# Performance work log

Hardware: AMD Instinct MI355X
Metric: run time of the kernel (lower is better)

The kernel has to match this reference:

```python
import jax, jax.numpy as jnp
import numpy as np

TAG_THR = 0.1
MIN_HEIGHT = 0.0
PULL_WEIGHT = 1.0
PUSH_WEIGHT = 1.0
EPS = 1e-6


def _bbox_iou(boxes):
    # boxes: [N,4] -> IoU [N,N] (standard, no +1 offset; heights in the loss
    # are also computed without +1)
    x1, y1, x2, y2 = boxes[:, 0], boxes[:, 1], boxes[:, 2], boxes[:, 3]
    area = (x2 - x1) * (y2 - y1)
    iw = jnp.clip(jnp.minimum(x2[:, None], x2[None, :]) - jnp.maximum(x1[:, None], x1[None, :]), 0.0)
    ih = jnp.clip(jnp.minimum(y2[:, None], y2[None, :]) - jnp.maximum(y1[:, None], y1[None, :]), 0.0)
    inter = iw * ih
    union = area[:, None] + area[None, :] - inter
    return inter / jnp.maximum(union, 1e-12)


def _single_image(pred, gt_inds, proposals):
    # pred [N,D], gt_inds [N] int, proposals [N,5]
    N = pred.shape[0]
    heights = proposals[:, 3] - proposals[:, 1]
    valid = (gt_inds >= 0) & (heights > MIN_HEIGHT)
    scores = proposals[:, 4]
    iou = _bbox_iou(proposals[:, :4])  # [N,N]

    def step(state, _):
        alive, tot_pull, tot_push, pull_cnt, push_cnt = state
        active = jnp.sum(alive) >= 2  # pop i; if nothing remains, the torch loop breaks
        # i = highest-scoring remaining proposal (greedy, score-sorted)
        i = jnp.argmax(jnp.where(alive, scores, -jnp.inf))
        rem = alive.at[i].set(False)
        overlap = (iou[i] > 0.0) & rem
        diff = jnp.mean((pred - pred[i]) ** 2, axis=1)  # [N]
        check = diff < TAG_THR
        same = gt_inds == gt_inds[i]
        pull_m = overlap & same & ~check
        push_m = overlap & ~same & check
        pn = jnp.sum(pull_m)
        qn = jnp.sum(push_m)
        pull_l = jnp.sum(jnp.where(pull_m, diff * scores, 0.0)) / jnp.maximum(pn, 1).astype(diff.dtype)
        push_l = jnp.sum(jnp.where(push_m, jnp.exp(-diff) * scores, 0.0)) / jnp.maximum(qn, 1).astype(diff.dtype)
        add_pull = active & (pn > 0)
        add_push = active & (qn > 0)
        tot_pull = tot_pull + jnp.where(add_pull, pull_l, 0.0)
        tot_push = tot_push + jnp.where(add_push, push_l, 0.0)
        pull_cnt = pull_cnt + add_pull.astype(jnp.float32)
        push_cnt = push_cnt + add_push.astype(jnp.float32)
        # suppress everything overlapping i whose tag is already close (diff < thr)
        new_alive = rem & ~(overlap & check)
        alive = jnp.where(active, new_alive, alive)
        return (alive, tot_pull, tot_push, pull_cnt, push_cnt), None

    z = jnp.float32(0.0)
    init = (valid, z, z, z, z)
    (_, tot_pull, tot_push, pull_cnt, push_cnt), _ = jax.lax.scan(step, init, None, length=N)
    pull = tot_pull / (pull_cnt + EPS)
    push = tot_push / (push_cnt + EPS)
    return push, pull


def setup_inputs() -> dict:
    key = jax.random.key(0)
    k1, k2, k3, k4, k5, k6, k7 = jax.random.split(key, 7)
    IMGS, N, D = 4, 2000, 4
    pred = jax.random.normal(k1, (IMGS, N, D), dtype=jnp.float32)
    gt_inds = jax.random.randint(k2, (IMGS, N), 0, 50, dtype=jnp.int32)
    x1 = jax.random.uniform(k3, (IMGS, N), minval=0.0, maxval=800.0)
    y1 = jax.random.uniform(k4, (IMGS, N), minval=0.0, maxval=800.0)
    w = jax.random.uniform(k5, (IMGS, N), minval=8.0, maxval=128.0)
    h = jax.random.uniform(k6, (IMGS, N), minval=8.0, maxval=128.0)
    score = jax.random.uniform(k7, (IMGS, N), minval=0.0, maxval=1.0)
    proposals = jnp.stack([x1, y1, x1 + w, y1 + h, score], axis=-1).astype(jnp.float32)
    gt_bboxes = jax.random.uniform(jax.random.fold_in(key, 9), (IMGS, 20, 4), dtype=jnp.float32)
    return {"pred": pred, "gt_inds": gt_inds, "proposals": proposals, "gt_bboxes": gt_bboxes}


def reference(pred, gt_inds, proposals, gt_bboxes):
    # gt_bboxes is accepted by the torch forward but never used in the loss math.
    push, pull = jax.vmap(_single_image)(pred, gt_inds, proposals)  # per-image scalars
    img_num = pred.shape[0]
    push_loss = jnp.sum(push) / img_num * PUSH_WEIGHT
    pull_loss = jnp.sum(pull) / img_num * PULL_WEIGHT
    return push_loss, pull_loss
```

## Files before the change

kernel.cpp:

```cpp
#include <hip/hip_runtime.h>
#include <stdint.h>

#define BLOCK 256
#define KMAX 8
#define NWAVES (BLOCK / 64)
#define S2 2048
#define NW 32
#define NCH 32
#define SPB 16
#define PB (S2 / SPB)
#define RB (S2 / BLOCK)
#define PCAP 65536
#define LDSP 6144
#define EFF_INF 0x7FFFFFFF

__device__ inline int rank_of(const unsigned long long* ss, int j) {
    int jw = j >> 6, jb = j & 63;
    int rk = __popcll(ss[jw] & (jb ? (~0ull >> (64 - jb)) : 0ull));
    for (int w = 0; w < jw; ++w) rk += __popcll(ss[w]);
    return rk;
}

__global__ __launch_bounds__(BLOCK) void rankcount_kernel(
    const float* __restrict__ proposals,
    int* __restrict__ partial, int* __restrict__ pcnt, int N, int imgs)
{
    const int bi = blockIdx.x, bj = blockIdx.y, img = blockIdx.z;
    const int t = threadIdx.x;
    if (bi == 0 && bj == 0 && t == 0) pcnt[img] = 0;
    const float* P = proposals + (size_t)img * N * 5;
    __shared__ unsigned sj[BLOCK];
    const int jbase = bj * BLOCK;
    {
        int j = jbase + t;
        sj[t] = (j < N) ? __float_as_uint(P[j*5 + 4]) : 0u;
    }
    __syncthreads();
    const int i = bi * BLOCK + t;
    if (i >= N) return;
    const unsigned my = __float_as_uint(P[i*5 + 4]);
    int p = 0;
    const uint4* s4 = (const uint4*)sj;
#pragma unroll
    for (int q = 0; q < BLOCK/4; ++q) {
        uint4 v = s4[q];
        int jj = jbase + q*4;
        p += (int)((v.x > my) | ((v.x == my) & (jj + 0 < i)));
        p += (int)((v.y > my) | ((v.y == my) & (jj + 1 < i)));
        p += (int)((v.z > my) | ((v.z == my) & (jj + 2 < i)));
        p += (int)((v.w > my) | ((v.w == my) & (jj + 3 < i)));
    }
    partial[((size_t)(img*RB + bj))*S2 + i] = p;
}

__global__ __launch_bounds__(BLOCK) void rankscatter_kernel(
    const float* __restrict__ pred, const int* __restrict__ gt_inds,
    const float* __restrict__ proposals, const int* __restrict__ partial,
    float* __restrict__ soa, int* __restrict__ sgt, int N, int imgs)
{
    const int img = blockIdx.y, t = threadIdx.x;
    const int i = blockIdx.x * BLOCK + t;
    const size_t stride = (size_t)imgs * S2;
    const size_t base   = (size_t)img * S2;

    if (i >= N) {
        if (i < S2) {
#pragma unroll
            for (int a = 0; a < 9; ++a) soa[(size_t)a*stride + base + i] = 0.f;
            sgt[base + i] = -1;
        }
        return;
    }

    const float* P = proposals + (size_t)img * N * 5;
    const float* E = pred      + (size_t)img * N * 4;
    const int*   G = gt_inds   + (size_t)img * N;

    const float p0 = P[i*5+0], p1 = P[i*5+1], p2 = P[i*5+2],
                p3 = P[i*5+3], p4 = P[i*5+4];
    const float q0 = E[i*4+0], q1 = E[i*4+1], q2 = E[i*4+2], q3 = E[i*4+3];
    const int   gg = G[i];

    int p = 0;
#pragma unroll
    for (int b = 0; b < RB; ++b)
        p += partial[((size_t)(img*RB + b))*S2 + i];

    soa[0*stride + base + p] = p0;
    soa[1*stride + base + p] = p1;
    soa[2*stride + base + p] = p2;
    soa[3*stride + base + p] = p3;
    soa[4*stride + base + p] = p4;
    soa[5*stride + base + p] = q0;
    soa[6*stride + base + p] = q1;
    soa[7*stride + base + p] = q2;
    soa[8*stride + base + p] = q3;
    sgt[base + p] = gg;
}

__global__ __launch_bounds__(BLOCK) void suppairs_kernel(
    const float* __restrict__ soa, unsigned* __restrict__ pairs,
    int* __restrict__ pcnt, int N, int imgs)
{
    const int ic = blockIdx.x, jc = blockIdx.y, img = blockIdx.z;
    if (ic < jc) return;
    const int t = threadIdx.x, wave = t >> 6, lane = t & 63;
    const size_t stride = (size_t)imgs * S2, base = (size_t)img * S2;
    __shared__ float si[8][64];
    for (int idx = t; idx < 512; idx += BLOCK) {
        int f = idx >> 6, e = idx & 63;
        int a = (f < 4) ? f : f + 1;
        si[f][e] = soa[(size_t)a*stride + base + ic*64 + e];
    }
    __syncthreads();
    const int j = jc*64 + lane;
    const float jx1 = soa[0*stride+base+j], jy1 = soa[1*stride+base+j];
    const float jx2 = soa[2*stride+base+j], jy2 = soa[3*stride+base+j];
    const float j0  = soa[5*stride+base+j], j1  = soa[6*stride+base+j];
    const float j2  = soa[7*stride+base+j], j3  = soa[8*stride+base+j];
    const bool jin = (j < N);
    unsigned* PL = pairs + (size_t)img * PCAP;
    for (int ii = 0; ii < 16; ++ii) {
        int il = wave*16 + ii;
        int i  = ic*64 + il;
        float bx1 = si[0][il], by1 = si[1][il], bx2 = si[2][il], by2 = si[3][il];
        float f0  = si[4][il], f1  = si[5][il], f2  = si[6][il], f3  = si[7][il];
        bool s = false;
        if (jin && i < N && i > j) {
            float iw = fminf(jx2, bx2) - fmaxf(jx1, bx1);
            float ih = fminf(jy2, by2) - fmaxf(jy1, by1);
            if (iw > 0.f && ih > 0.f) {
                float d0 = j0-f0, d1 = j1-f1, d2 = j2-f2, d3 = j3-f3;
                float diff = 0.25f*(d0*d0 + d1*d1 + d2*d2 + d3*d3);
                s = diff < 0.1f;
            }
        }
        unsigned long long m = __ballot(s);
        if (m) {
            int leader = __ffsll((unsigned long long)m) - 1;
            int basei = 0;
            if (lane == leader) basei = atomicAdd(&pcnt[img], __popcll(m));
            basei = __shfl(basei, leader);
            if (s) {
                int idx = basei + __popcll(m & ((lane == 0) ? 0ull : (~0ull >> (64 - lane))));
                if (idx < PCAP) PL[idx] = ((unsigned)j << 11) | (unsigned)i;
            }
        }
    }
}

__global__ __launch_bounds__(64) void greedy_kernel(
    const unsigned* __restrict__ pairs, const int* __restrict__ pcnt,
    const int* __restrict__ sgt, const float* __restrict__ soa,
    unsigned long long* __restrict__ selw_out, int imgs)
{
    const int img = blockIdx.x, l = threadIdx.x;
    const size_t stride = (size_t)imgs * S2, base = (size_t)img * S2;
    __shared__ unsigned long long skilled[NW], ssel[NW], sloc[64];
    __shared__ unsigned spair[LDSP];

    int P = pcnt[img]; if (P > PCAP) P = PCAP;
    const unsigned* PL = pairs + (size_t)img * PCAP;
    const bool staged = (P <= LDSP);
    if (staged) for (int p = l; p < P; p += 64) spair[p] = PL[p];

    for (int c = 0; c < NCH; ++c) {
        const int j = c*64 + l;
        int g = sgt[base + j];
        float a = soa[1*stride + base + j];
        float b = soa[3*stride + base + j];
        bool invalid = !(g >= 0 && (b - a) > 0.f);
        unsigned long long bb = __ballot(invalid);
        if (l == 0) skilled[c] = bb;
    }
    __syncthreads();

    const unsigned long long lowmask = (l == 0) ? 0ull : (~0ull >> (64 - l));

    for (int c = 0; c < NCH; ++c) {
        sloc[l] = 0ull;
        __syncthreads();
        for (int p = l; p < P; p += 64) {
            unsigned v = staged ? spair[p] : PL[p];
            int lo = v >> 11, hi = v & 2047;
            if ((lo >> 6) == c && (hi >> 6) == c)
                atomicOr(&sloc[hi & 63], 1ull << (lo & 63));
        }
        __syncthreads();
        unsigned long long U = ~skilled[c];
        const unsigned long long loc = sloc[l];
        unsigned long long sel = 0ull;
        while (U) {
            bool inU = (U >> l) & 1ull;
            unsigned long long A = __ballot(inU && ((loc & U & lowmask) == 0ull));
            sel |= A;
            bool kill = inU && !((A >> l) & 1ull) && ((loc & A) != 0ull);
            unsigned long long K = __ballot(kill);
            U &= ~(A | K);
        }
        if (l == 0) ssel[c] = sel;
        if (sel != 0ull) {
            for (int p = l; p < P; p += 64) {
                unsigned v = staged ? spair[p] : PL[p];
                int lo = v >> 11, hi = v & 2047;
                if ((lo >> 6) == c && ((sel >> (lo & 63)) & 1ull) && (hi >> 6) > c)
                    atomicOr(&skilled[hi >> 6], 1ull << (hi & 63));
            }
        }
        __syncthreads();
    }
    if (l < NW) selw_out[(size_t)img*NW + l] = ssel[l];
}

__global__ __launch_bounds__(BLOCK) void effsteps_kernel(
    const unsigned* __restrict__ pairs, const int* __restrict__ pcnt,
    const unsigned long long* __restrict__ selw,
    const int* __restrict__ sgt, const float* __restrict__ soa,
    int* __restrict__ eff, int* __restrict__ nsteps, int imgs)
{
    const int img = blockIdx.x, t = threadIdx.x;
    const int lane = t & 63, wave = t >> 6;
    const size_t stride = (size_t)imgs * S2, base = (size_t)img * S2;
    __shared__ unsigned long long ss[NW];
    __shared__ int sistar[S2];
    __shared__ unsigned hist[S2];
    __shared__ int ints[2*NWAVES];
    __shared__ unsigned wsum[NWAVES];
    __shared__ int bm[NWAVES];
    if (t < NW) ss[t] = selw[(size_t)img*NW + t];
    for (int x = t; x < S2; x += BLOCK) { sistar[x] = EFF_INF; hist[x] = 0u; }
    __syncthreads();

    int P = pcnt[img]; if (P > PCAP) P = PCAP;
    const unsigned* PL = pairs + (size_t)img * PCAP;
    for (int p = t; p < P; p += BLOCK) {
        unsigned v = PL[p];
        int lo = v >> 11, hi = v & 2047;
        if ((ss[lo >> 6] >> (lo & 63)) & 1ull) atomicMin(&sistar[hi], lo);
    }
    __syncthreads();

    int myV = 0, mySc = 0;
#pragma unroll
    for (int k = 0; k < 8; ++k) {
        const int j = k*BLOCK + t;
        int g = sgt[base + j];
        float a = soa[1*stride+base+j], b = soa[3*stride+base+j];
        bool valid = (g >= 0) && ((b - a) > 0.f);
        bool selb  = (ss[j>>6] >> (j & 63)) & 1ull;
        int e;
        if (!valid) e = 0;
        else if (selb) { e = rank_of(ss, j); ++myV; ++mySc; }
        else {
            ++myV;
            int istar = sistar[j];
            if (istar == EFF_INF) e = EFF_INF;
            else { e = rank_of(ss, istar) + 1; atomicAdd(&hist[e - 1], 1u); }
        }
        eff[(size_t)img*S2 + j] = e;
    }
    __syncthreads();

    int v = myV, sc = mySc;
    for (int o = 32; o > 0; o >>= 1) { v += __shfl_down(v, o); sc += __shfl_down(sc, o); }
    if (lane == 0) { ints[wave] = v; ints[NWAVES + wave] = sc; }
    __syncthreads();
    int V = 0, Sc = 0;
    for (int w = 0; w < NWAVES; ++w) { V += ints[w]; Sc += ints[NWAVES + w]; }

    unsigned loc[8]; unsigned s = 0;
#pragma unroll
    for (int k = 0; k < 8; ++k) { s += hist[t*8 + k]; loc[k] = s; }
    unsigned tot = s;
    for (int o = 1; o < 64; o <<= 1) {
        unsigned u = __shfl_up(tot, o);
        if (lane >= o) tot += u;
    }
    if (lane == 63) wsum[wave] = tot;
    __syncthreads();
    unsigned woff = 0;
    for (int w = 0; w < wave; ++w) woff += wsum[w];
    unsigned exclP = woff + tot - s;
    __syncthreads();
#pragma unroll
    for (int k = 0; k < 8; ++k) hist[t*8 + k] = exclP + loc[k];
    __syncthreads();

    int best = EFF_INF;
    for (int r = t; r < Sc; r += BLOCK) {
        unsigned rem = (r == 0) ? 0u : hist[r - 1];
        int alive = V - r - (int)rem;
        if (alive < 2) best = min(best, r);
    }
    for (int o = 32; o > 0; o >>= 1) best = min(best, __shfl_down(best, o));
    if (lane == 0) bm[wave] = best;
    __syncthreads();
    if (t == 0) {
        int b = bm[0];
        for (int w = 1; w < NWAVES; ++w) b = min(b, bm[w]);
        nsteps[img] = min(b, Sc);
    }
}

__global__ __launch_bounds__(BLOCK) void pairs_kernel(
    const float* __restrict__ soa, const int* __restrict__ sgt,
    const int* __restrict__ eff, const unsigned long long* __restrict__ selw,
    const int* __restrict__ nsteps, float* __restrict__ partials, int imgs)
{
    const int ic = blockIdx.x, img = blockIdx.y;
    const int t = threadIdx.x, wave = t >> 6, lane = t & 63;
    const size_t stride = (size_t)imgs * S2, base = (size_t)img * S2;
    __shared__ unsigned long long ss[NW];
    __shared__ float pw[NWAVES][4];
    __shared__ int anyact;
    if (t < NW) ss[t] = selw[(size_t)img*NW + t];
    if (t == 0) anyact = 0;
    __syncthreads();
    const int ns = nsteps[img];

    float bx1[4], by1[4], bx2[4], by2[4], f0[4], f1[4], f2[4], f3[4];
    int bgt[4], rk[4]; bool act[4];
    bool any = false;
#pragma unroll
    for (int u = 0; u < 4; ++u) {
        const int i = ic*SPB + wave*4 + u;
        bool selb = (ss[i>>6] >> (i & 63)) & 1ull;
        int r = rank_of(ss, i);
        rk[u] = r;
        act[u] = selb && (r < ns);
        any |= act[u];
        if (act[u]) {
            bx1[u] = soa[0*stride+base+i]; by1[u] = soa[1*stride+base+i];
            bx2[u] = soa[2*stride+base+i]; by2[u] = soa[3*stride+base+i];
            f0[u]  = soa[5*stride+base+i]; f1[u]  = soa[6*stride+base+i];
            f2[u]  = soa[7*stride+base+i]; f3[u]  = soa[8*stride+base+i];
            bgt[u] = sgt[base + i];
        } else {
            bx1[u]=by1[u]=bx2[u]=by2[u]=0.f; f0[u]=f1[u]=f2[u]=f3[u]=0.f; bgt[u]=-2;
        }
    }
    if (any && lane == 0) anyact = 1;
    __syncthreads();
    if (!anyact) {
        if (t < 4) partials[((size_t)img*PB + ic)*4 + t] = 0.f;
        return;
    }

    float ps[4] = {0,0,0,0}, pn[4] = {0,0,0,0}, qs[4] = {0,0,0,0}, qn[4] = {0,0,0,0};
    for (int jt = 0; jt < NCH; ++jt) {
        const int j = jt*64 + lane;
        const float jx1 = soa[0*stride+base+j], jy1 = soa[1*stride+base+j];
        const float jx2 = soa[2*stride+base+j], jy2 = soa[3*stride+base+j];
        const float jsc = soa[4*stride+base+j];
        const float j0  = soa[5*stride+base+j], j1  = soa[6*stride+base+j];
        const float j2  = soa[7*stride+base+j], j3  = soa[8*stride+base+j];
        const int   jgt = sgt[base + j];
        const int   jef = eff[(size_t)img*S2 + j];
#pragma unroll
        for (int u = 0; u < 4; ++u) {
            if (!act[u]) continue;
            if (rk[u] < jef) {
                float iw = fminf(jx2, bx2[u]) - fmaxf(jx1, bx1[u]);
                float ih = fminf(jy2, by2[u]) - fmaxf(jy1, by1[u]);
                if (iw > 0.f && ih > 0.f) {
                    float d0 = j0 - f0[u], d1 = j1 - f1[u];
                    float d2 = j2 - f2[u], d3 = j3 - f3[u];
                    float diff = 0.25f*(d0*d0 + d1*d1 + d2*d2 + d3*d3);
                    bool check = diff < 0.1f;
                    bool same  = (jgt == bgt[u]);
                    if (same && !check)      { ps[u] += diff * jsc;       pn[u] += 1.f; }
                    else if (!same && check) { qs[u] += expf(-diff)*jsc;  qn[u] += 1.f; }
                }
            }
        }
    }

    float sPull = 0.f, cPull = 0.f, sPush = 0.f, cPush = 0.f;
#pragma unroll
    for (int u = 0; u < 4; ++u) {
        if (!act[u]) continue;
        float a0 = ps[u], a1 = pn[u], a2 = qs[u], a3 = qn[u];
        for (int o = 32; o > 0; o >>= 1) {
            a0 += __shfl_down(a0, o); a1 += __shfl_down(a1, o);
            a2 += __shfl_down(a2, o); a3 += __shfl_down(a3, o);
        }
        if (lane == 0) {
            if (a1 > 0.f) { sPull += a0 / a1; cPull += 1.f; }
            if (a3 > 0.f) { sPush += a2 / a3; cPush += 1.f; }
        }
    }
    if (lane == 0) {
        pw[wave][0] = sPull; pw[wave][1] = cPull;
        pw[wave][2] = sPush; pw[wave][3] = cPush;
    }
    __syncthreads();
    if (t == 0) {
        float a = 0, b = 0, c = 0, d = 0;
        for (int w = 0; w < NWAVES; ++w) {
            a += pw[w][0]; b += pw[w][1]; c += pw[w][2]; d += pw[w][3];
        }
        float* p = partials + ((size_t)img*PB + ic)*4;
        p[0] = a; p[1] = b; p[2] = c; p[3] = d;
    }
}

__global__ __launch_bounds__(BLOCK) void finalize_kernel(
    const float* __restrict__ partials, float* __restrict__ out, int imgs)
{
    const int t = threadIdx.x;
    __shared__ float a[8][4];
    if (t < 32) ((float*)a)[t] = 0.f;
    __syncthreads();
    for (int e = t; e < imgs * PB; e += BLOCK) {
        int img = e / PB;
        const float* p = partials + (size_t)e * 4;
#pragma unroll
        for (int k = 0; k < 4; ++k) {
            float v = p[k];
            if (v != 0.f) atomicAdd(&a[img][k], v);
        }
    }
    __syncthreads();
    if (t == 0) {
        float push = 0.f, pull = 0.f;
        for (int i = 0; i < imgs; ++i) {
            pull += a[i][0] / (a[i][1] + 1e-6f);
            push += a[i][2] / (a[i][3] + 1e-6f);
        }
        out[0] = push / (float)imgs;
        out[1] = pull / (float)imgs;
    }
}

__global__ __launch_bounds__(BLOCK) void tagloss_kernel(
    const float* __restrict__ pred, const int* __restrict__ gt_inds,
    const float* __restrict__ proposals, float* __restrict__ ws, int N)
{
    const int img = blockIdx.x, t = threadIdx.x;
    const int lane = t & 63, wav = t >> 6;
    const float* P = proposals + (size_t)img * N * 5;
    const float* E = pred      + (size_t)img * N * 4;
    const int*   G = gt_inds   + (size_t)img * N;
    float x1[KMAX], y1[KMAX], x2[KMAX], y2[KMAX], sc[KMAX];
    float e0[KMAX], e1[KMAX], e2[KMAX], e3[KMAX];
    int gt[KMAX]; unsigned amask = 0u; int local_alive = 0;
#pragma unroll
    for (int k = 0; k < KMAX; ++k) {
        int j = k * BLOCK + t;
        if (j < N) {
            x1[k]=P[j*5+0]; y1[k]=P[j*5+1]; x2[k]=P[j*5+2]; y2[k]=P[j*5+3]; sc[k]=P[j*5+4];
            e0[k]=E[j*4+0]; e1[k]=E[j*4+1]; e2[k]=E[j*4+2]; e3[k]=E[j*4+3]; gt[k]=G[j];
            if (gt[k] >= 0 && (y2[k]-y1[k]) > 0.0f) { amask |= 1u<<k; local_alive++; }
        } else { x1[k]=y1[k]=x2[k]=y2[k]=0.f; sc[k]=0.f; e0[k]=e1[k]=e2[k]=e3[k]=0.f; gt[k]=-1; }
    }
    __shared__ unsigned long long s_key[NWAVES];
    __shared__ float s_b[9];
    __shared__ float s_part[NWAVES][5];
    int alive_count;
    {
        float v = (float)local_alive;
#pragma unroll
        for (int o = 32; o > 0; o >>= 1) v += __shfl_down(v, o);
        if (lane == 0) s_part[wav][0] = v;
        __syncthreads();
        float tot = 0.f;
        for (int w = 0; w < NWAVES; ++w) tot += s_part[w][0];
        alive_count = (int)tot;
    }
    float tot_pull=0.f, tot_push=0.f, pull_cnt=0.f, push_cnt=0.f;
    while (alive_count >= 2) {
        unsigned long long key = 0ull;
#pragma unroll
        for (int k = 0; k < KMAX; ++k)
            if (amask & (1u<<k)) {
                unsigned long long kk = ((unsigned long long)__float_as_uint(sc[k])<<32)
                                      | (unsigned long long)(0xFFFFFFFFu - (unsigned)(k*BLOCK+t));
                if (kk > key) key = kk;
            }
#pragma unroll
        for (int o = 32; o > 0; o >>= 1) {
            unsigned long long ok = __shfl_down(key, o);
            if (ok > key) key = ok;
        }
        if (lane == 0) s_key[wav] = key;
        __syncthreads();
        unsigned long long bk = s_key[0];
        for (int w = 1; w < NWAVES; ++w) if (s_key[w] > bk) bk = s_key[w];
        const int i = (int)(0xFFFFFFFFu - (unsigned)(bk & 0xFFFFFFFFull));
        if ((i & (BLOCK-1)) == t) {
            int k = i / BLOCK;
            s_b[0]=x1[k]; s_b[1]=y1[k]; s_b[2]=x2[k]; s_b[3]=y2[k];
            s_b[4]=e0[k]; s_b[5]=e1[k]; s_b[6]=e2[k]; s_b[7]=e3[k];
            s_b[8]=__int_as_float(gt[k]);
        }
        __syncthreads();
        const float bx1=s_b[0], by1=s_b[1], bx2=s_b[2], by2=s_b[3];
        const float f0=s_b[4], f1=s_b[5], f2=s_b[6], f3=s_b[7];
        const int bgt = __float_as_int(s_b[8]);
        const float areai = (bx2-bx1)*(by2-by1);
        float psum=0.f,qsum=0.f,pn=0.f,qn=0.f,scnt=0.f;
#pragma unroll
        for (int k = 0; k < KMAX; ++k) {
            if (!(amask & (1u<<k))) continue;
            int j = k*BLOCK+t;
            if (j == i) { amask &= ~(1u<<k); continue; }
            float iw = fmaxf(fminf(x2[k],bx2)-fmaxf(x1[k],bx1),0.f);
            float ih = fmaxf(fminf(y2[k],by2)-fmaxf(y1[k],by1),0.f);
            float inter = iw*ih;
            float uni = (x2[k]-x1[k])*(y2[k]-y1[k]) + areai - inter;
            float iou = inter / fmaxf(uni, 1e-12f);
            if (iou > 0.f) {
                float d0=e0[k]-f0,d1=e1[k]-f1,d2=e2[k]-f2,d3=e3[k]-f3;
                float diff = 0.25f*(d0*d0+d1*d1+d2*d2+d3*d3);
                bool check = diff < 0.1f;
                bool same = (gt[k]==bgt);
                if (same && !check) { psum += diff*sc[k]; pn += 1.f; }
                if (!same && check) { qsum += __expf(-diff)*sc[k]; qn += 1.f; }
                if (check)          { amask &= ~(1u<<k); scnt += 1.f; }
            }
        }
        float r0=psum,r1=pn,r2=qsum,r3=qn,r4=scnt;
#pragma unroll
        for (int o = 32; o > 0; o >>= 1) {
            r0+=__shfl_down(r0,o); r1+=__shfl_down(r1,o); r2+=__shfl_down(r2,o);
            r3+=__shfl_down(r3,o); r4+=__shfl_down(r4,o);
        }
        if (lane == 0) { s_part[wav][0]=r0;s_part[wav][1]=r1;s_part[wav][2]=r2;s_part[wav][3]=r3;s_part[wav][4]=r4; }
        __syncthreads();
        float T0=0,T1=0,T2=0,T3=0,T4=0;
        for (int w = 0; w < NWAVES; ++w) {
            T0+=s_part[w][0];T1+=s_part[w][1];T2+=s_part[w][2];T3+=s_part[w][3];T4+=s_part[w][4];
        }
        if (T1 > 0.f) { tot_pull += T0/T1; pull_cnt += 1.f; }
        if (T3 > 0.f) { tot_push += T2/T3; push_cnt += 1.f; }
        alive_count -= 1 + (int)T4;
    }
    if (t == 0) {
        ws[img*2+0] = tot_push / (push_cnt + 1e-6f);
        ws[img*2+1] = tot_pull / (pull_cnt + 1e-6f);
    }
}

__global__ void finalize_fb_kernel(const float* __restrict__ ws,
                                   float* __restrict__ out, int imgs)
{
    if (threadIdx.x == 0 && blockIdx.x == 0) {
        float push = 0.f, pull = 0.f;
        for (int k = 0; k < imgs; ++k) { push += ws[2*k]; pull += ws[2*k+1]; }
        out[0] = push / (float)imgs;
        out[1] = pull / (float)imgs;
    }
}

extern "C" void kernel_launch(void* const* d_in, const int* in_sizes, int n_in,
                              void* d_out, int out_size, void* d_ws, size_t ws_size,
                              hipStream_t stream) {
    const float* pred      = (const float*)d_in[0];
    const int*   gt_inds   = (const int*)  d_in[1];
    const float* proposals = (const float*)d_in[2];
    const int imgs = in_sizes[3] / 80;
    const int N    = in_sizes[1] / imgs;

    size_t off = 0;
    auto alloc = [&](size_t b) { size_t o = off; off += (b + 255) & ~(size_t)255; return o; };
    const size_t soa_off  = alloc((size_t)9 * imgs * S2 * 4);
    const size_t sgt_off  = alloc((size_t)imgs * S2 * 4);
    const size_t sel_off  = alloc((size_t)imgs * NW * 8);
    const size_t eff_off  = alloc((size_t)imgs * S2 * 4);
    const size_t nst_off  = alloc((size_t)imgs * 4);
    const size_t par_off  = alloc((size_t)imgs * PB * 16);
    const size_t rnk_off  = alloc((size_t)imgs * RB * S2 * 4);
    const size_t prs_off  = alloc((size_t)imgs * PCAP * 4);
    const size_t pcn_off  = alloc((size_t)imgs * 4);
    const size_t need = off;

    if (N <= S2 && imgs <= 8 && ws_size >= need) {
        char* w = (char*)d_ws;
        float*              soa  = (float*)(w + soa_off);
        int*                sgt  = (int*)(w + sgt_off);
        unsigned long long* sel  = (unsigned long long*)(w + sel_off);
        int*                eff  = (int*)(w + eff_off);
        int*                nst  = (int*)(w + nst_off);
        float*              par  = (float*)(w + par_off);
        int*                rnk  = (int*)(w + rnk_off);
        unsigned*           prs  = (unsigned*)(w + prs_off);
        int*                pcn  = (int*)(w + pcn_off);

        rankcount_kernel<<<dim3(RB, RB, imgs), BLOCK, 0, stream>>>(
            proposals, rnk, pcn, N, imgs);
        rankscatter_kernel<<<dim3(RB, imgs), BLOCK, 0, stream>>>(
            pred, gt_inds, proposals, rnk, soa, sgt, N, imgs);
        suppairs_kernel<<<dim3(NCH, NCH, imgs), BLOCK, 0, stream>>>(
            soa, prs, pcn, N, imgs);
        greedy_kernel<<<imgs, 64, 0, stream>>>(prs, pcn, sgt, soa, sel, imgs);
        effsteps_kernel<<<imgs, BLOCK, 0, stream>>>(prs, pcn, sel, sgt, soa,
                                                    eff, nst, imgs);
        pairs_kernel<<<dim3(PB, imgs), BLOCK, 0, stream>>>(soa, sgt, eff, sel,
                                                           nst, par, imgs);
        finalize_kernel<<<1, BLOCK, 0, stream>>>(par, (float*)d_out, imgs);
    } else {
        float* ws = (float*)d_ws;
        tagloss_kernel<<<imgs, BLOCK, 0, stream>>>(pred, gt_inds, proposals, ws, N);
        finalize_fb_kernel<<<1, 64, 0, stream>>>(ws, (float*)d_out, imgs);
    }
}
```

Baseline: 175.1 us.

## Pre-bucket overlap pairs by chunk in greedy kernel to avoid per-chunk rescans

The greedy kernel used to rescan the whole pair list twice per 64-wide chunk, once to build the local conflict masks and once to propagate kills. It now makes a single pass that builds all intra-chunk masks in a 2048-entry LDS array and sorts cross-chunk pairs into per-chunk LDS buckets of fixed capacity. Each chunk then reads only its own bucket, and falls back to a global scan when a bucket overflows. This raises LDS use and lowers the staging threshold, and it assumes pairs are stored with lo<hi, as the old `(hi>>6) > c` filter implied.

```diff
diff --git a/kernel.cpp b/kernel.cpp
--- a/kernel.cpp
+++ b/kernel.cpp
@@ -11,7 +11,8 @@
 #define PB (S2 / SPB)
 #define RB (S2 / BLOCK)
 #define PCAP 65536
-#define LDSP 6144
+#define LDSP2 4096
+#define BCAP 64
 #define EFF_INF 0x7FFFFFFF
 
 __device__ inline int rank_of(const unsigned long long* ss, int j) {
@@ -156,12 +157,18 @@
 {
     const int img = blockIdx.x, l = threadIdx.x;
     const size_t stride = (size_t)imgs * S2, base = (size_t)img * S2;
-    __shared__ unsigned long long skilled[NW], ssel[NW], sloc[64];
-    __shared__ unsigned spair[LDSP];
+    __shared__ unsigned long long slocAll[S2];
+    __shared__ unsigned spair[LDSP2];
+    __shared__ unsigned bucket[NCH * BCAP];
+    __shared__ int bcnt[NCH];
+    __shared__ unsigned long long skilled[NW], ssel[NW];
 
     int P = pcnt[img]; if (P > PCAP) P = PCAP;
     const unsigned* PL = pairs + (size_t)img * PCAP;
-    const bool staged = (P <= LDSP);
+    const bool staged = (P <= LDSP2);
+
+    for (int x = l; x < S2; x += 64) slocAll[x] = 0ull;
+    if (l < NCH) bcnt[l] = 0;
     if (staged) for (int p = l; p < P; p += 64) spair[p] = PL[p];
 
     for (int c = 0; c < NCH; ++c) {
@@ -175,20 +182,23 @@
     }
     __syncthreads();
 
+    for (int p = l; p < P; p += 64) {
+        unsigned v = staged ? spair[p] : PL[p];
+        int lo = v >> 11, hi = v & 2047;
+        if ((lo >> 6) == (hi >> 6)) {
+            atomicOr(&slocAll[hi], 1ull << (lo & 63));
+        } else {
+            int idx = atomicAdd(&bcnt[lo >> 6], 1);
+            if (idx < BCAP) bucket[(lo >> 6)*BCAP + idx] = v;
+        }
+    }
+    __syncthreads();
+
     const unsigned long long lowmask = (l == 0) ? 0ull : (~0ull >> (64 - l));
 
     for (int c = 0; c < NCH; ++c) {
-        sloc[l] = 0ull;
-        __syncthreads();
-        for (int p = l; p < P; p += 64) {
-            unsigned v = staged ? spair[p] : PL[p];
-            int lo = v >> 11, hi = v & 2047;
-            if ((lo >> 6) == c && (hi >> 6) == c)
-                atomicOr(&sloc[hi & 63], 1ull << (lo & 63));
-        }
-        __syncthreads();
         unsigned long long U = ~skilled[c];
-        const unsigned long long loc = sloc[l];
+        const unsigned long long loc = slocAll[c*64 + l];
         unsigned long long sel = 0ull;
         while (U) {
             bool inU = (U >> l) & 1ull;
@@ -200,11 +210,22 @@
         }
         if (l == 0) ssel[c] = sel;
         if (sel != 0ull) {
-            for (int p = l; p < P; p += 64) {
-                unsigned v = staged ? spair[p] : PL[p];
-                int lo = v >> 11, hi = v & 2047;
-                if ((lo >> 6) == c && ((sel >> (lo & 63)) & 1ull) && (hi >> 6) > c)
-                    atomicOr(&skilled[hi >> 6], 1ull << (hi & 63));
+            const int bc = bcnt[c];
+            if (bc <= BCAP) {
+                for (int q = l; q < bc; q += 64) {
+                    unsigned v = bucket[c*BCAP + q];
+                    int lo = v >> 11, hi = v & 2047;
+                    if ((sel >> (lo & 63)) & 1ull)
+                        atomicOr(&skilled[hi >> 6], 1ull << (hi & 63));
+                }
+            } else {
+                for (int p = l; p < P; p += 64) {
+                    unsigned v = PL[p];
+                    int lo = v >> 11, hi = v & 2047;
+                    if ((lo >> 6) == c && (hi >> 6) != c &&
+                        ((sel >> (lo & 63)) & 1ull))
+                        atomicOr(&skilled[hi >> 6], 1ull << (hi & 63));
+                }
             }
         }
         __syncthreads();
```

Result: faster. 152.1 us (-13.2%).
